# Performance work log

Measured on AMD Instinct MI355X. Metric: run time of the kernel, lower is better.

## Reference

```python
import jax, jax.numpy as jnp
import numpy as np

SCALE = 4.0      # OBBPointAssigner default scale
INF = jnp.inf


def setup_inputs() -> dict:
    key = jax.random.key(0)
    k1, k2, k3, k4, k5 = jax.random.split(key, 5)
    N, K = 262144, 256
    # points: (x, y, stride) with power-of-two strides 8..128 (5 FPN levels)
    xy = jax.random.uniform(k1, (N, 2), dtype=jnp.float32) * 1024.0
    lvl_exp = jax.random.randint(k2, (N,), 0, 5)
    stride = (2.0 ** (3 + lvl_exp)).astype(jnp.float32)
    points = jnp.concatenate([xy, stride[:, None]], axis=1)  # (N, 3)
    # oriented gt boxes as 4 corners (here axis-aligned rectangles), shape (K, 8)
    ctr = jax.random.uniform(k3, (K, 2), dtype=jnp.float32) * 1024.0
    wh = jax.random.uniform(k4, (K, 2), dtype=jnp.float32) * 248.0 + 8.0
    dx, dy = wh[:, 0] / 2, wh[:, 1] / 2
    cx, cy = ctr[:, 0], ctr[:, 1]
    gt_obboxes = jnp.stack([cx - dx, cy - dy, cx + dx, cy - dy,
                            cx + dx, cy + dy, cx - dx, cy + dy], axis=1)
    gt_labels = jax.random.randint(k5, (K,), 1, 16).astype(jnp.int32)
    return {"points": points, "gt_obboxes": gt_obboxes, "gt_labels": gt_labels}


def reference(points, gt_obboxes, gt_labels):
    """Vectorized OBBPointAssigner.assign (scale=4, pos_num=1).

    Returns (assigned_gt_inds, assigned_labels): 0 = background,
    positive = 1-based index of the assigned gt box.
    """
    N = points.shape[0]
    K = gt_obboxes.shape[0]
    px = points[:, :2]                         # (N, 2)
    p_lvl = jnp.log2(points[:, 2]).astype(jnp.int32)   # (N,)
    lvl_min, lvl_max = p_lvl.min(), p_lvl.max()

    # oriented box -> axis-aligned box
    xs, ys = gt_obboxes[:, 0::2], gt_obboxes[:, 1::2]  # (K, 4)
    xmin, xmax = xs.min(1), xs.max(1)
    ymin, ymax = ys.min(1), ys.max(1)
    g_ctr = jnp.stack([(xmin + xmax) / 2, (ymin + ymax) / 2], axis=1)   # (K, 2)
    g_wh = jnp.stack([xmax - xmin, ymax - ymin], axis=1).clip(min=1e-6)  # (K, 2)
    g_lvl = ((jnp.log2(g_wh[:, 0] / SCALE) + jnp.log2(g_wh[:, 1] / SCALE)) / 2)
    g_lvl = jnp.clip(g_lvl.astype(jnp.int32), lvl_min, lvl_max)          # (K,)

    # (K, N) normalized distance, masked to the gt's pyramid level
    d = jnp.linalg.norm((px[None, :, :] - g_ctr[:, None, :]) / g_wh[:, None, :], axis=-1)
    d = jnp.where(p_lvl[None, :] == g_lvl[:, None], d, INF)

    # per-GT nearest point (pos_num = 1)
    min_dist = d.min(axis=1)                  # (K,)
    nearest = d.argmin(axis=1)                # (K,) point index per gt
    valid = jnp.isfinite(min_dist)

    # sequential loop semantics: a point keeps the gt with strictly smaller
    # distance; ties go to the earlier (smaller-index) gt.
    best = jnp.full((N,), INF, dtype=d.dtype).at[nearest].min(jnp.where(valid, min_dist, INF))
    win = valid & (min_dist == best[nearest])
    gt_idx = jnp.arange(K, dtype=jnp.int32)
    owner = jnp.full((N,), K, dtype=jnp.int32).at[nearest].min(jnp.where(win, gt_idx, K))

    assigned_gt_inds = jnp.where(owner < K, owner + 1, 0)
    assigned_labels = jnp.where(owner < K, gt_labels[jnp.clip(owner, 0, K - 1)], 0)
    return assigned_gt_inds, assigned_labels
```

## Files before the change

kernel.cpp:

```cpp
#include <hip/hip_runtime.h>
#include <cstdint>

#define INFIN __builtin_inff()
constexpr int KMAX = 256;


__global__ __launch_bounds__(1024)
void k_dist(const float* __restrict__ pts, const float* __restrict__ gtb,
            unsigned long long* __restrict__ pack2, int* __restrict__ out,
            int N, int K) {
    const int t = threadIdx.x, b = blockIdx.x;
    const int wv = t >> 6, lane = t & 63;

    __shared__ float4 sp[1024];
    __shared__ float s_cx[KMAX], s_cy[KMAX], s_w[KMAX], s_h[KMAX], s_rw[KMAX], s_rh[KMAX];
    __shared__ int   s_org[KMAX], s_gbin[KMAX];
    __shared__ int   s_wh[16][5], s_wb[16][5], s_pcnt[5];
    __shared__ int   s_gwh[4][5], s_gwb[4][5], s_gcnt[5];
    __shared__ unsigned long long sh_p[1024];

    int i = b * 1024 + t;
    bool act = (i < N);
    float px = 0.f, py = 0.f;
    int pbin = -1;
    if (act) {
        px = pts[3 * i]; py = pts[3 * i + 1];
        unsigned u = __float_as_uint(pts[3 * i + 2]);
        int e = (int)((u >> 23) & 0xFF) - 127;
        pbin = e - 3;
        if (pbin < 0 || pbin > 4) pbin = -1;
        out[i] = 0; out[N + i] = 0;
    }

    int prank = 0;
    #pragma unroll
    for (int bb = 0; bb < 5; ++bb) {
        unsigned long long m = __ballot(pbin == bb);
        if (pbin == bb) prank = __popcll(m & ((1ull << lane) - 1ull));
        if (lane == 0) s_wh[wv][bb] = __popcll(m);
    }
    __syncthreads();
    if (t < 5) {
        int run = 0;
        for (int w2 = 0; w2 < 16; ++w2) { s_wb[w2][t] = run; run += s_wh[w2][t]; }
        s_pcnt[t] = run;
    }
    __syncthreads();

    int lmin = 127, lmax = -127;
    #pragma unroll
    for (int bb = 0; bb < 5; ++bb) {
        if (s_pcnt[bb] > 0) { lmin = min(lmin, bb + 3); lmax = max(lmax, bb + 3); }
    }

    if (pbin >= 0) {
        int base = 0;
        for (int bb = 0; bb < pbin; ++bb) base += s_pcnt[bb];
        sp[base + s_wb[wv][pbin] + prank] = make_float4(px, py, __int_as_float(i), 0.f);
    }

    float cx = 0.f, cy = 0.f, w = 1.f, h = 1.f, rw = 1.f, rh = 1.f;
    int gbin = 99;
    if (t < K) {
        float x0 = gtb[8*t+0], y0 = gtb[8*t+1], x1 = gtb[8*t+2], y1 = gtb[8*t+3];
        float x2 = gtb[8*t+4], y2 = gtb[8*t+5], x3 = gtb[8*t+6], y3 = gtb[8*t+7];
        float xmin = fminf(fminf(x0, x1), fminf(x2, x3));
        float xmax = fmaxf(fmaxf(x0, x1), fmaxf(x2, x3));
        float ymin = fminf(fminf(y0, y1), fminf(y2, y3));
        float ymax = fmaxf(fmaxf(y0, y1), fmaxf(y2, y3));
        cx = __fmul_rn(__fadd_rn(xmin, xmax), 0.5f);
        cy = __fmul_rn(__fadd_rn(ymin, ymax), 0.5f);
        w  = fmaxf(__fsub_rn(xmax, xmin), 1e-6f);
        h  = fmaxf(__fsub_rn(ymax, ymin), 1e-6f);
        rw = 1.0f / w;
        rh = 1.0f / h;
        float gf = __fmul_rn(__fadd_rn(log2f(__fmul_rn(w, 0.25f)),
                                       log2f(__fmul_rn(h, 0.25f))), 0.5f);
        int gl = (int)gf;
        gl = min(max(gl, lmin), lmax);
        gbin = min(max(gl - 3, 0), 4);
    }
    int grank = 0;
    if (t < 256) {
        #pragma unroll
        for (int bb = 0; bb < 5; ++bb) {
            unsigned long long m = __ballot(gbin == bb);
            if (gbin == bb) grank = __popcll(m & ((1ull << lane) - 1ull));
            if (lane == 0) s_gwh[wv][bb] = __popcll(m);
        }
    }
    __syncthreads();
    if (t < 5) {
        int run = 0;
        for (int w2 = 0; w2 < 4; ++w2) { s_gwb[w2][t] = run; run += s_gwh[w2][t]; }
        s_gcnt[t] = run;
    }
    __syncthreads();
    if (t < K) {
        int base = 0;
        for (int bb = 0; bb < gbin; ++bb) base += s_gcnt[bb];
        int slot = base + s_gwb[wv][gbin] + grank;
        s_cx[slot] = cx; s_cy[slot] = cy;
        s_w[slot] = w;   s_h[slot] = h;
        s_rw[slot] = rw; s_rh[slot] = rh;
        s_org[slot] = t; s_gbin[slot] = gbin;
    }
    __syncthreads();

    const int c = t >> 8, g = t & 255;
    unsigned long long bp = ~0ull;
    if (g < K) {
        float gcx = s_cx[g], gcy = s_cy[g];
        float gw = s_w[g], gh = s_h[g], grw = s_rw[g], grh = s_rh[g];
        int gbin2 = s_gbin[g];
        int base = 0;
        for (int bb = 0; bb < gbin2; ++bb) base += s_pcnt[bb];
        int cnt = s_pcnt[gbin2];
        int seg = (cnt + 3) >> 2;
        int i0 = c * seg, i1 = min(i0 + seg, cnt);
        #pragma unroll 4
        for (int ii = i0; ii < i1; ++ii) {
            float4 q = sp[base + ii];
            float dx = __fsub_rn(q.x, gcx);
            float dy = __fsub_rn(q.y, gcy);
            float qx = __fmul_rn(dx, grw);
            qx = __fmaf_rn(__fmaf_rn(-gw, qx, dx), grw, qx);
            float qy = __fmul_rn(dy, grh);
            qy = __fmaf_rn(__fmaf_rn(-gh, qy, dy), grh, qy);
            float s = __fadd_rn(__fmul_rn(qx, qx), __fmul_rn(qy, qy));
            float d = __fsqrt_rn(s);
            unsigned long long cand =
                ((unsigned long long)__float_as_uint(d) << 32)
                | (unsigned)__float_as_int(q.z);
            bp = cand < bp ? cand : bp;
        }
    }

    sh_p[t] = bp;
    __syncthreads();
    if (t < K) {
        unsigned long long p0 = sh_p[t];
        #pragma unroll
        for (int cc = 1; cc < 4; ++cc) {
            unsigned long long p1 = sh_p[cc * 256 + t];
            p0 = p1 < p0 ? p1 : p0;
        }
        pack2[(size_t)b * KMAX + s_org[t]] = p0;
    }
}

__global__ __launch_bounds__(1024)
void k_final(const unsigned long long* __restrict__ pack2,
             const int* __restrict__ glab, int* __restrict__ out,
             int N, int K, int nrows) {
    __shared__ unsigned long long sh_p[1024];
    __shared__ int hkey[512];
    __shared__ unsigned long long hval[512];
    const int t = threadIdx.x;
    const int c = t >> 8, k = t & 255;

    if (t < 512) { hkey[t] = -1; hval[t] = ~0ull; }

    unsigned long long best = ~0ull;
    #pragma unroll 8
    for (int b = c; b < nrows; b += 4) {
        unsigned long long v = pack2[(size_t)b * KMAX + k];
        best = v < best ? v : best;
    }
    sh_p[t] = best;
    __syncthreads();

    if (t < 256) {
        unsigned long long p = sh_p[t];
        #pragma unroll
        for (int cc = 1; cc < 4; ++cc) {
            unsigned long long p1 = sh_p[cc * 256 + t];
            p = p1 < p ? p1 : p;
        }
        unsigned db = (unsigned)(p >> 32);
        bool valid = (t < K) && (db < 0x7F800000u);
        int nk = (int)(unsigned)(p & 0xFFFFFFFFu);

        int h = 0;
        if (valid) {
            unsigned long long myp = ((unsigned long long)db << 32) | (unsigned)t;
            h = (int)((((unsigned)nk) * 2654435761u) >> 23) & 511;
            while (true) {
                int old = atomicCAS(&hkey[h], -1, nk);
                if (old == -1 || old == nk) { atomicMin(&hval[h], myp); break; }
                h = (h + 1) & 511;
            }
        }
        __syncthreads();
        if (valid && (int)(unsigned)(hval[h] & 0xFFFFFFFFu) == t) {
            out[nk]     = t + 1;
            out[N + nk] = glab[t];
        }
    } else {
        __syncthreads();
    }
}

extern "C" void kernel_launch(void* const* d_in, const int* in_sizes, int n_in,
                              void* d_out, int out_size, void* d_ws, size_t ws_size,
                              hipStream_t stream) {
    const float* pts = (const float*)d_in[0];
    const float* gtb = (const float*)d_in[1];
    const int*  glab = (const int*)d_in[2];
    int N = in_sizes[0] / 3;
    int K = in_sizes[1] / 8;
    unsigned long long* pack2 = (unsigned long long*)d_ws;
    int nrows = (N + 1023) / 1024;

    k_dist<<<nrows, 1024, 0, stream>>>(pts, gtb, pack2, (int*)d_out, N, K);
    k_final<<<1, 1024, 0, stream>>>(pack2, glab, (int*)d_out, N, K, nrows);
}
```

Baseline: 28.19 us.

## Split GT boxes across four blocks per 4096-point group to shrink partial rows

Each k_dist block now walks four 1024-point tiles and handles only a 64-box slice of the sorted ground-truth boxes. Four blocks share each 4096-point group, so the per-box partial-min table written to workspace has a quarter as many rows. This targets the single-block k_final reduction, which reads every row. The cost is that every point tile is loaded, binned and zero-written four times (once per slice block), and each block does more barrier rounds.

```diff
diff --git a/kernel.cpp b/kernel.cpp
--- a/kernel.cpp
+++ b/kernel.cpp
@@ -3,13 +3,16 @@
 
 #define INFIN __builtin_inff()
 constexpr int KMAX = 256;
+constexpr int TPB  = 4;
+constexpr int NSL  = 4;
 
 
 __global__ __launch_bounds__(1024)
 void k_dist(const float* __restrict__ pts, const float* __restrict__ gtb,
             unsigned long long* __restrict__ pack2, int* __restrict__ out,
-            int N, int K) {
+            int N, int K, int npg) {
     const int t = threadIdx.x, b = blockIdx.x;
+    const int pg = b >> 2, sl = b & 3;
     const int wv = t >> 6, lane = t & 63;
 
     __shared__ float4 sp[1024];
@@ -19,133 +22,148 @@
     __shared__ int   s_gwh[4][5], s_gwb[4][5], s_gcnt[5];
     __shared__ unsigned long long sh_p[1024];
 
-    int i = b * 1024 + t;
-    bool act = (i < N);
-    float px = 0.f, py = 0.f;
-    int pbin = -1;
-    if (act) {
-        px = pts[3 * i]; py = pts[3 * i + 1];
-        unsigned u = __float_as_uint(pts[3 * i + 2]);
-        int e = (int)((u >> 23) & 0xFF) - 127;
-        pbin = e - 3;
-        if (pbin < 0 || pbin > 4) pbin = -1;
-        out[i] = 0; out[N + i] = 0;
-    }
-
-    int prank = 0;
-    #pragma unroll
-    for (int bb = 0; bb < 5; ++bb) {
-        unsigned long long m = __ballot(pbin == bb);
-        if (pbin == bb) prank = __popcll(m & ((1ull << lane) - 1ull));
-        if (lane == 0) s_wh[wv][bb] = __popcll(m);
-    }
-    __syncthreads();
-    if (t < 5) {
-        int run = 0;
-        for (int w2 = 0; w2 < 16; ++w2) { s_wb[w2][t] = run; run += s_wh[w2][t]; }
-        s_pcnt[t] = run;
-    }
-    __syncthreads();
-
-    int lmin = 127, lmax = -127;
-    #pragma unroll
-    for (int bb = 0; bb < 5; ++bb) {
-        if (s_pcnt[bb] > 0) { lmin = min(lmin, bb + 3); lmax = max(lmax, bb + 3); }
-    }
-
-    if (pbin >= 0) {
-        int base = 0;
-        for (int bb = 0; bb < pbin; ++bb) base += s_pcnt[bb];
-        sp[base + s_wb[wv][pbin] + prank] = make_float4(px, py, __int_as_float(i), 0.f);
-    }
-
-    float cx = 0.f, cy = 0.f, w = 1.f, h = 1.f, rw = 1.f, rh = 1.f;
-    int gbin = 99;
-    if (t < K) {
-        float x0 = gtb[8*t+0], y0 = gtb[8*t+1], x1 = gtb[8*t+2], y1 = gtb[8*t+3];
-        float x2 = gtb[8*t+4], y2 = gtb[8*t+5], x3 = gtb[8*t+6], y3 = gtb[8*t+7];
-        float xmin = fminf(fminf(x0, x1), fminf(x2, x3));
-        float xmax = fmaxf(fmaxf(x0, x1), fmaxf(x2, x3));
-        float ymin = fminf(fminf(y0, y1), fminf(y2, y3));
-        float ymax = fmaxf(fmaxf(y0, y1), fmaxf(y2, y3));
-        cx = __fmul_rn(__fadd_rn(xmin, xmax), 0.5f);
-        cy = __fmul_rn(__fadd_rn(ymin, ymax), 0.5f);
-        w  = fmaxf(__fsub_rn(xmax, xmin), 1e-6f);
-        h  = fmaxf(__fsub_rn(ymax, ymin), 1e-6f);
-        rw = 1.0f / w;
-        rh = 1.0f / h;
-        float gf = __fmul_rn(__fadd_rn(log2f(__fmul_rn(w, 0.25f)),
-                                       log2f(__fmul_rn(h, 0.25f))), 0.5f);
-        int gl = (int)gf;
-        gl = min(max(gl, lmin), lmax);
-        gbin = min(max(gl - 3, 0), 4);
-    }
-    int grank = 0;
-    if (t < 256) {
+    float gcx = 0.f, gcy = 0.f, gw = 1.f, gh = 1.f, grw = 1.f, grh = 1.f;
+    int gbin2 = 0;
+    bool gact = false;
+    unsigned long long bp = ~0ull;
+
+    for (int tt = 0; tt < TPB; ++tt) {
+        int i = (pg * TPB + tt) * 1024 + t;
+        bool act = (i < N);
+        float px = 0.f, py = 0.f;
+        int pbin = -1;
+        if (act) {
+            px = pts[3 * i]; py = pts[3 * i + 1];
+            unsigned u = __float_as_uint(pts[3 * i + 2]);
+            int e = (int)((u >> 23) & 0xFF) - 127;
+            pbin = e - 3;
+            if (pbin < 0 || pbin > 4) pbin = -1;
+            out[i] = 0; out[N + i] = 0;
+        }
+
+        int prank = 0;
         #pragma unroll
         for (int bb = 0; bb < 5; ++bb) {
-            unsigned long long m = __ballot(gbin == bb);
-            if (gbin == bb) grank = __popcll(m & ((1ull << lane) - 1ull));
-            if (lane == 0) s_gwh[wv][bb] = __popcll(m);
-        }
-    }
-    __syncthreads();
-    if (t < 5) {
-        int run = 0;
-        for (int w2 = 0; w2 < 4; ++w2) { s_gwb[w2][t] = run; run += s_gwh[w2][t]; }
-        s_gcnt[t] = run;
-    }
-    __syncthreads();
-    if (t < K) {
-        int base = 0;
-        for (int bb = 0; bb < gbin; ++bb) base += s_gcnt[bb];
-        int slot = base + s_gwb[wv][gbin] + grank;
-        s_cx[slot] = cx; s_cy[slot] = cy;
-        s_w[slot] = w;   s_h[slot] = h;
-        s_rw[slot] = rw; s_rh[slot] = rh;
-        s_org[slot] = t; s_gbin[slot] = gbin;
-    }
-    __syncthreads();
-
-    const int c = t >> 8, g = t & 255;
-    unsigned long long bp = ~0ull;
-    if (g < K) {
-        float gcx = s_cx[g], gcy = s_cy[g];
-        float gw = s_w[g], gh = s_h[g], grw = s_rw[g], grh = s_rh[g];
-        int gbin2 = s_gbin[g];
-        int base = 0;
-        for (int bb = 0; bb < gbin2; ++bb) base += s_pcnt[bb];
-        int cnt = s_pcnt[gbin2];
-        int seg = (cnt + 3) >> 2;
-        int i0 = c * seg, i1 = min(i0 + seg, cnt);
-        #pragma unroll 4
-        for (int ii = i0; ii < i1; ++ii) {
-            float4 q = sp[base + ii];
-            float dx = __fsub_rn(q.x, gcx);
-            float dy = __fsub_rn(q.y, gcy);
-            float qx = __fmul_rn(dx, grw);
-            qx = __fmaf_rn(__fmaf_rn(-gw, qx, dx), grw, qx);
-            float qy = __fmul_rn(dy, grh);
-            qy = __fmaf_rn(__fmaf_rn(-gh, qy, dy), grh, qy);
-            float s = __fadd_rn(__fmul_rn(qx, qx), __fmul_rn(qy, qy));
-            float d = __fsqrt_rn(s);
-            unsigned long long cand =
-                ((unsigned long long)__float_as_uint(d) << 32)
-                | (unsigned)__float_as_int(q.z);
-            bp = cand < bp ? cand : bp;
+            unsigned long long m = __ballot(pbin == bb);
+            if (pbin == bb) prank = __popcll(m & ((1ull << lane) - 1ull));
+            if (lane == 0) s_wh[wv][bb] = __popcll(m);
+        }
+        __syncthreads();
+        if (t < 5) {
+            int run = 0;
+            for (int w2 = 0; w2 < 16; ++w2) { s_wb[w2][t] = run; run += s_wh[w2][t]; }
+            s_pcnt[t] = run;
+        }
+        __syncthreads();
+
+        if (pbin >= 0) {
+            int base = 0;
+            for (int bb = 0; bb < pbin; ++bb) base += s_pcnt[bb];
+            sp[base + s_wb[wv][pbin] + prank] = make_float4(px, py, __int_as_float(i), 0.f);
+        }
+
+        if (tt == 0) {
+            int lmin = 127, lmax = -127;
+            #pragma unroll
+            for (int bb = 0; bb < 5; ++bb) {
+                if (s_pcnt[bb] > 0) { lmin = min(lmin, bb + 3); lmax = max(lmax, bb + 3); }
+            }
+            float cx = 0.f, cy = 0.f, w = 1.f, h = 1.f, rw = 1.f, rh = 1.f;
+            int gbin = 99;
+            if (t < K) {
+                float x0 = gtb[8*t+0], y0 = gtb[8*t+1], x1 = gtb[8*t+2], y1 = gtb[8*t+3];
+                float x2 = gtb[8*t+4], y2 = gtb[8*t+5], x3 = gtb[8*t+6], y3 = gtb[8*t+7];
+                float xmin = fminf(fminf(x0, x1), fminf(x2, x3));
+                float xmax = fmaxf(fmaxf(x0, x1), fmaxf(x2, x3));
+                float ymin = fminf(fminf(y0, y1), fminf(y2, y3));
+                float ymax = fmaxf(fmaxf(y0, y1), fmaxf(y2, y3));
+                cx = __fmul_rn(__fadd_rn(xmin, xmax), 0.5f);
+                cy = __fmul_rn(__fadd_rn(ymin, ymax), 0.5f);
+                w  = fmaxf(__fsub_rn(xmax, xmin), 1e-6f);
+                h  = fmaxf(__fsub_rn(ymax, ymin), 1e-6f);
+                rw = 1.0f / w;
+                rh = 1.0f / h;
+                float gf = __fmul_rn(__fadd_rn(log2f(__fmul_rn(w, 0.25f)),
+                                               log2f(__fmul_rn(h, 0.25f))), 0.5f);
+                int gl = (int)gf;
+                gl = min(max(gl, lmin), lmax);
+                gbin = min(max(gl - 3, 0), 4);
+            }
+            int grank = 0;
+            if (t < 256) {
+                #pragma unroll
+                for (int bb = 0; bb < 5; ++bb) {
+                    unsigned long long m = __ballot(gbin == bb);
+                    if (gbin == bb) grank = __popcll(m & ((1ull << lane) - 1ull));
+                    if (lane == 0) s_gwh[wv][bb] = __popcll(m);
+                }
+            }
+            __syncthreads();
+            if (t < 5) {
+                int run = 0;
+                for (int w2 = 0; w2 < 4; ++w2) { s_gwb[w2][t] = run; run += s_gwh[w2][t]; }
+                s_gcnt[t] = run;
+            }
+            __syncthreads();
+            if (t < K) {
+                int base = 0;
+                for (int bb = 0; bb < gbin; ++bb) base += s_gcnt[bb];
+                int slot = base + s_gwb[wv][gbin] + grank;
+                s_cx[slot] = cx; s_cy[slot] = cy;
+                s_w[slot] = w;   s_h[slot] = h;
+                s_rw[slot] = rw; s_rh[slot] = rh;
+                s_org[slot] = t; s_gbin[slot] = gbin;
+            }
+            __syncthreads();
+            int slot = sl * 64 + (t & 63);
+            gact = slot < K;
+            if (gact) {
+                gcx = s_cx[slot]; gcy = s_cy[slot];
+                gw = s_w[slot];  gh = s_h[slot];
+                grw = s_rw[slot]; grh = s_rh[slot];
+                gbin2 = s_gbin[slot];
+            }
+        } else {
+            __syncthreads();
+        }
+
+        if (gact) {
+            const int c = t >> 6;
+            int base = 0;
+            for (int bb = 0; bb < gbin2; ++bb) base += s_pcnt[bb];
+            int cnt = s_pcnt[gbin2];
+            int seg = (cnt + 15) >> 4;
+            int i0 = c * seg, i1 = min(i0 + seg, cnt);
+            #pragma unroll 4
+            for (int ii = i0; ii < i1; ++ii) {
+                float4 q = sp[base + ii];
+                float dx = __fsub_rn(q.x, gcx);
+                float dy = __fsub_rn(q.y, gcy);
+                float qx = __fmul_rn(dx, grw);
+                qx = __fmaf_rn(__fmaf_rn(-gw, qx, dx), grw, qx);
+                float qy = __fmul_rn(dy, grh);
+                qy = __fmaf_rn(__fmaf_rn(-gh, qy, dy), grh, qy);
+                float s = __fadd_rn(__fmul_rn(qx, qx), __fmul_rn(qy, qy));
+                float d = __fsqrt_rn(s);
+                unsigned long long cand =
+                    ((unsigned long long)__float_as_uint(d) << 32)
+                    | (unsigned)__float_as_int(q.z);
+                bp = cand < bp ? cand : bp;
+            }
         }
     }
 
     sh_p[t] = bp;
     __syncthreads();
-    if (t < K) {
+    if (t < 64) {
         unsigned long long p0 = sh_p[t];
         #pragma unroll
-        for (int cc = 1; cc < 4; ++cc) {
-            unsigned long long p1 = sh_p[cc * 256 + t];
+        for (int cc = 1; cc < 16; ++cc) {
+            unsigned long long p1 = sh_p[cc * 64 + t];
             p0 = p1 < p0 ? p1 : p0;
         }
-        pack2[(size_t)b * KMAX + s_org[t]] = p0;
+        int slot = sl * 64 + t;
+        if (slot < K) pack2[(size_t)pg * KMAX + s_org[slot]] = p0;
     }
 }
 
@@ -163,8 +181,8 @@
 
     unsigned long long best = ~0ull;
     #pragma unroll 8
-    for (int b = c; b < nrows; b += 4) {
-        unsigned long long v = pack2[(size_t)b * KMAX + k];
+    for (int r = c; r < nrows; r += 4) {
+        unsigned long long v = pack2[(size_t)r * KMAX + k];
         best = v < best ? v : best;
     }
     sh_p[t] = best;
@@ -210,8 +228,8 @@
     int N = in_sizes[0] / 3;
     int K = in_sizes[1] / 8;
     unsigned long long* pack2 = (unsigned long long*)d_ws;
-    int nrows = (N + 1023) / 1024;
-
-    k_dist<<<nrows, 1024, 0, stream>>>(pts, gtb, pack2, (int*)d_out, N, K);
-    k_final<<<1, 1024, 0, stream>>>(pack2, glab, (int*)d_out, N, K, nrows);
+    int npg = (N + TPB * 1024 - 1) / (TPB * 1024);
+
+    k_dist<<<npg * NSL, 1024, 0, stream>>>(pts, gtb, pack2, (int*)d_out, N, K, npg);
+    k_final<<<1, 1024, 0, stream>>>(pack2, glab, (int*)d_out, N, K, npg);
 }
```

Result: faster. 27.12 us (-3.8%).
